# Kernel tuning notes

Measured on AMD Instinct MI355X. Metric: run time of the kernel, lower is better.

The kernel has to match this reference:

```python
import jax, jax.numpy as jnp
import numpy as np

B, T = 64, 64
H = 256
CLIP = 0.2


def _conv(x, W, b, s):
    y = jax.lax.conv_general_dilated(x, W, (s, s), 'VALID',
                                     dimension_numbers=('NHWC', 'HWIO', 'NHWC'))
    return jax.nn.leaky_relu(y + b, negative_slope=0.2)


def _lstm(x, Wk, Wr, b):
    # keras LSTM, gate order i,f,g,o; x: (B,T,256) -> (B,T,256)
    h0 = jnp.zeros((x.shape[0], H), x.dtype)

    def step(carry, xt):
        h, c = carry
        z = xt @ Wk + h @ Wr + b
        i, f, g, o = jnp.split(z, 4, axis=-1)
        c = jax.nn.sigmoid(f) * c + jax.nn.sigmoid(i) * jnp.tanh(g)
        h = jax.nn.sigmoid(o) * jnp.tanh(c)
        return (h, c), h

    _, hs = jax.lax.scan(step, (h0, h0), jnp.swapaxes(x, 0, 1))
    return jnp.swapaxes(hs, 0, 1)


def setup_inputs():
    key = jax.random.key(0)
    ks = jax.random.split(key, 24)
    s = 0.05
    x = jax.random.normal(ks[0], (B, T, 13, 8, 8), jnp.float32)
    a_taken = jax.random.randint(ks[1], (B, T), 0, 36)
    mask = jax.random.randint(ks[2], (B, T, 4096), 0, 2).astype(jnp.int32)
    # taken actions must be legal (mask=1), as in real rollouts
    bi = jnp.repeat(jnp.arange(B), T)
    ti = jnp.tile(jnp.arange(T), B)
    mask = mask.at[bi, ti, a_taken.reshape(-1)].set(1)
    lg_prob_old = -jnp.abs(jax.random.normal(ks[3], (B, T), jnp.float32)) - 1.0
    GAE = jax.random.normal(ks[4], (B, T), jnp.float32)
    old_v_pred = jax.random.normal(ks[5], (B, T), jnp.float32)
    returns = jax.random.normal(ks[6], (B, T), jnp.float32)
    return {
        'x': x, 'mask': mask, 'lg_prob_old': lg_prob_old, 'a_taken': a_taken,
        'GAE': GAE, 'old_v_pred': old_v_pred, 'returns': returns,
        'W1': jax.random.normal(ks[7], (2, 2, 8, 16), jnp.float32) * s,
        'b1': jnp.zeros((16,), jnp.float32),
        'W2': jax.random.normal(ks[8], (2, 2, 16, 32), jnp.float32) * s,
        'b2': jnp.zeros((32,), jnp.float32),
        'W3': jax.random.normal(ks[9], (2, 2, 32, 64), jnp.float32) * s,
        'b3': jnp.zeros((64,), jnp.float32),
        'W4': jax.random.normal(ks[10], (1, 1, 64, 128), jnp.float32) * s,
        'b4': jnp.zeros((128,), jnp.float32),
        'lstm_k': jax.random.normal(ks[11], (256, 1024), jnp.float32) * s,
        'lstm_r': jax.random.normal(ks[12], (256, 1024), jnp.float32) * s,
        'lstm_b': jnp.zeros((1024,), jnp.float32),
        'pir_W': jax.random.normal(ks[13], (256, 36), jnp.float32) * s,
        'pir_b': jnp.zeros((36,), jnp.float32),
        'pim_W': jax.random.normal(ks[14], (256, 4096), jnp.float32) * s,
        'pim_b': jnp.zeros((4096,), jnp.float32),
        'v_W': jax.random.normal(ks[15], (256, 1), jnp.float32) * s,
        'v_b': jnp.zeros((1,), jnp.float32),
    }


def reference(x, mask, lg_prob_old, a_taken, GAE, old_v_pred, returns,
              W1, b1, W2, b2, W3, b3, W4, b4,
              lstm_k, lstm_r, lstm_b, pir_W, pir_b, pim_W, pim_b, v_W, v_b):
    Bn, Tn = x.shape[0], x.shape[1]
    h = x.reshape(Bn * Tn, 13, 8, 8)  # NHWC: H=13, W=8, C=8
    h = _conv(h, W1, b1, 2)  # (BT,6,4,16)
    h = _conv(h, W2, b2, 1)  # (BT,5,3,32)
    h = _conv(h, W3, b3, 2)  # (BT,2,1,64)
    h = _conv(h, W4, b4, 1)  # (BT,2,1,128)
    # keras Flatten(data_format='channels_first') permutes dim1 to last then flattens
    h = jnp.transpose(h, (0, 2, 3, 1)).reshape(Bn, Tn, -1)  # (B,T,256)
    lstm = _lstm(h, lstm_k, lstm_r, lstm_b).reshape(-1, H)  # (BT,256)

    pir = jax.nn.softmax(lstm @ pir_W + pir_b, axis=-1)  # (BT,36)
    maskf = mask.reshape(-1, 4096).astype(jnp.float32)
    pim = jax.nn.softmax(lstm @ pim_W + pim_b, axis=-1) * maskf
    scale = jnp.sum(pim, axis=1, keepdims=True)
    pim = pim / jnp.where(scale > 0, scale, jnp.ones_like(scale))  # (BT,4096)
    vpred = lstm @ v_W + v_b  # (BT,1)

    lg_old = lg_prob_old.reshape(-1)
    a = a_taken.reshape(-1)
    gae = GAE.reshape(-1)
    ovp = old_v_pred.reshape(-1)
    ret = returns.reshape(-1)
    gae = (gae - jnp.mean(gae)) / (jnp.std(gae) + 1e-8)

    t = jnp.arange(a.shape[0])
    p = jnp.where(t % 2 == 0, pir[t, a], pim[t, a])  # alternating heads
    lg_new = jnp.log(p)
    rt = jnp.exp(lg_new - lg_old)
    pg1 = -gae * rt
    pg2 = -gae * jnp.clip(rt, 1.0 - CLIP, 1.0 + CLIP)
    pg_loss = jnp.mean(jnp.maximum(pg1, pg2))

    # faithful to original TF: (BT,1) vpred broadcast against (BT,) -> (BT,BT)
    vpredclipped = ovp + jnp.clip(vpred - ovp, -CLIP, CLIP)
    vf1 = jnp.square(vpred - ret)
    vf2 = jnp.square(vpredclipped - ret)
    vf_loss = 0.5 * jnp.mean(jnp.maximum(vf1, vf2))

    pim_e = pim + (1.0 - maskf)
    entropy = -jnp.sum(pir * jnp.log(pir)) - jnp.sum(pim_e * jnp.log(pim_e))
    loss = pg_loss - entropy + vf_loss
    return (loss, pg_loss, entropy, vf_loss)
```

## Files before the change

kernel.cpp:

```cpp
#include <hip/hip_runtime.h>

typedef unsigned short u16;
typedef unsigned int   u32;

#define BT   4096
#define TSEQ 64
#define NB   64

typedef __attribute__((ext_vector_type(8))) short  short8;
typedef __attribute__((ext_vector_type(4))) float  f32x4;
typedef __attribute__((ext_vector_type(2))) _Float16 h2;

__device__ __forceinline__ float bf(u16 v) {
    u32 u = ((u32)v) << 16;
    return __builtin_bit_cast(float, u);
}
__device__ __forceinline__ u16 f2b(float f) {
    u32 u = __builtin_bit_cast(u32, f);
    return (u16)((u + 0x7fffu + ((u >> 16) & 1u)) >> 16);
}
__device__ __forceinline__ float lrelu(float x) { return x > 0.f ? x : 0.2f * x; }
__device__ __forceinline__ h2 i2h(int v) { return __builtin_bit_cast(h2, v); }
__device__ __forceinline__ float dot2(int hbits, int wbits, float acc) {
#if __has_builtin(__builtin_amdgcn_fdot2)
    return __builtin_amdgcn_fdot2(i2h(hbits), i2h(wbits), acc, false);
#else
    h2 a = i2h(hbits), b = i2h(wbits);
    return acc + (float)a.x * (float)b.x + (float)a.y * (float)b.y;
#endif
}
__device__ __forceinline__ float fsigm(float x) { return 1.f / (1.f + __expf(-x)); }
__device__ __forceinline__ float ftanh(float x) { return 1.f - 2.f / (__expf(2.f * x) + 1.f); }
__device__ __forceinline__ float ldf(const void* p, int i, int f32) {
    return f32 ? ((const float*)p)[i] : bf(((const u16*)p)[i]);
}
__device__ __forceinline__ u16 ldb(const void* p, int i, int f32) {
    return f32 ? f2b(((const float*)p)[i]) : ((const u16*)p)[i];
}

struct PrepPtrs {
    const void *x, *W1, *b1, *W2, *b2, *W3, *b3, *W4, *b4;
    const void *Wr, *Wk, *Wpim, *Wpir, *Wv;
    const u16* probe;
    u16 *featbf, *PF, *PBk, *PBpim, *PBpir;
    float* scal; int* flag;
};

#define PACK_BLKS 6208
#define CONV_BLKS 2048

__global__ __launch_bounds__(256) void prep_kernel(PrepPtrs P)
{
    const int bid = blockIdx.x, tid = threadIdx.x;
    const int lane = tid & 63;
    u16 pv = P.probe[2 * lane];
    int e = (pv >> 7) & 0xFF;
    unsigned long long m = __ballot(pv == 0 || (e >= 100 && e <= 130));
    const int f32 = (__popcll(m) < 48) ? 1 : 0;

    if (bid == 0 && tid < 32) { P.scal[tid] = 0.f; if (tid == 0) *P.flag = f32; }

    if (bid < PACK_BLKS) {
        const int blk = bid;
        if (blk < 1024) {
            int gid = blk * 256 + tid;
            int k = gid >> 10, col = gid & 1023;
            float f = ldf(P.Wr, gid, f32);
            _Float16 h = (_Float16)f;
            P.PF[((size_t)(k >> 3) * 1024 + col) * 8 + (k & 7)] =
                __builtin_bit_cast(unsigned short, h);
        } else if (blk < 2048) {
            int gid = (blk - 1024) * 256 + tid;
            int k = gid >> 10, col = gid & 1023;
            P.PBk[((((size_t)(k >> 5) << 10) + col) * 4 + ((k >> 3) & 3)) * 8 + (k & 7)] =
                ldb(P.Wk, gid, f32);
        } else if (blk < 6144) {
            int gid = (blk - 2048) * 256 + tid;
            int k = gid >> 12, col = gid & 4095;
            P.PBpim[((((size_t)(k >> 5) << 12) + col) * 4 + ((k >> 3) & 3)) * 8 + (k & 7)] =
                ldb(P.Wpim, gid, f32);
        } else {
            int gid = (blk - 6144) * 256 + tid;
            int k = gid >> 6, col = gid & 63;
            u16 v = 0;
            if (col < 36)      v = ldb(P.Wpir, k * 36 + col, f32);
            else if (col == 36) v = ldb(P.Wv, k, f32);
            P.PBpir[(((size_t)(k >> 5) * 64 + col) * 4 + ((k >> 3) & 3)) * 8 + (k & 7)] = v;
        }
        return;
    }

    __shared__ __align__(16) u16 wl[19184];
    __shared__ float xs[2][832];
    __shared__ float c1[2][384];
    __shared__ float c2[2][480];
    __shared__ float c3[2][128];
    const int pair = bid - PACK_BLKS;
    const int sub = tid >> 7, stid = tid & 127;
    const int bt = pair * 2 + sub;

    {
        const void* sp[8] = {P.W1, P.b1, P.W2, P.b2, P.W3, P.b3, P.W4, P.b4};
        const int   sn[8] = {512, 16, 2048, 32, 8192, 64, 8192, 128};
        int o = 0;
        for (int s = 0; s < 8; s++) {
            for (int i = tid; i < sn[s]; i += 256) wl[o + i] = ldb(sp[s], i, f32);
            o += sn[s];
        }
    }
    for (int i = stid; i < 832; i += 128) xs[sub][i] = ldf(P.x, bt * 832 + i, f32);
    __syncthreads();

    for (int idx = stid; idx < 96; idx += 128) {
        int pos = idx >> 2, g = idx & 3;
        int oh = pos >> 2, ow = pos & 3;
        float a0 = bf(wl[512 + g * 4]), a1 = bf(wl[513 + g * 4]),
              a2 = bf(wl[514 + g * 4]), a3 = bf(wl[515 + g * 4]);
        for (int kh = 0; kh < 2; kh++)
            for (int kw = 0; kw < 2; kw++)
#pragma unroll
                for (int ic = 0; ic < 8; ic++) {
                    float xv = xs[sub][(2 * oh + kh) * 64 + (2 * ow + kw) * 8 + ic];
                    ushort4 w = *(const ushort4*)&wl[((kh * 2 + kw) * 8 + ic) * 16 + g * 4];
                    a0 += xv * bf(w.x); a1 += xv * bf(w.y);
                    a2 += xv * bf(w.z); a3 += xv * bf(w.w);
                }
        c1[sub][pos * 16 + g * 4]     = lrelu(a0);
        c1[sub][pos * 16 + g * 4 + 1] = lrelu(a1);
        c1[sub][pos * 16 + g * 4 + 2] = lrelu(a2);
        c1[sub][pos * 16 + g * 4 + 3] = lrelu(a3);
    }
    __syncthreads();

    for (int idx = stid; idx < 120; idx += 128) {
        int pos = idx >> 3, g = idx & 7;
        int oh = pos / 3, ow = pos % 3;
        float a0 = bf(wl[2576 + g * 4]), a1 = bf(wl[2577 + g * 4]),
              a2 = bf(wl[2578 + g * 4]), a3 = bf(wl[2579 + g * 4]);
        for (int kh = 0; kh < 2; kh++)
            for (int kw = 0; kw < 2; kw++)
#pragma unroll
                for (int ic = 0; ic < 16; ic++) {
                    float xv = c1[sub][((oh + kh) * 4 + (ow + kw)) * 16 + ic];
                    ushort4 w = *(const ushort4*)&wl[528 + ((kh * 2 + kw) * 16 + ic) * 32 + g * 4];
                    a0 += xv * bf(w.x); a1 += xv * bf(w.y);
                    a2 += xv * bf(w.z); a3 += xv * bf(w.w);
                }
        c2[sub][pos * 32 + g * 4]     = lrelu(a0);
        c2[sub][pos * 32 + g * 4 + 1] = lrelu(a1);
        c2[sub][pos * 32 + g * 4 + 2] = lrelu(a2);
        c2[sub][pos * 32 + g * 4 + 3] = lrelu(a3);
    }
    __syncthreads();

    for (int idx = stid; idx < 32; idx += 128) {
        int oh = idx >> 4, g = idx & 15;
        float a0 = bf(wl[10800 + g * 4]), a1 = bf(wl[10801 + g * 4]),
              a2 = bf(wl[10802 + g * 4]), a3 = bf(wl[10803 + g * 4]);
        for (int kh = 0; kh < 2; kh++)
            for (int kw = 0; kw < 2; kw++)
#pragma unroll
                for (int ic = 0; ic < 32; ic++) {
                    float xv = c2[sub][((2 * oh + kh) * 3 + kw) * 32 + ic];
                    ushort4 w = *(const ushort4*)&wl[2608 + ((kh * 2 + kw) * 32 + ic) * 64 + g * 4];
                    a0 += xv * bf(w.x); a1 += xv * bf(w.y);
                    a2 += xv * bf(w.z); a3 += xv * bf(w.w);
                }
        c3[sub][oh * 64 + g * 4]     = lrelu(a0);
        c3[sub][oh * 64 + g * 4 + 1] = lrelu(a1);
        c3[sub][oh * 64 + g * 4 + 2] = lrelu(a2);
        c3[sub][oh * 64 + g * 4 + 3] = lrelu(a3);
    }
    __syncthreads();

    for (int idx = stid; idx < 64; idx += 128) {
        int oh = idx >> 5, g = idx & 31;
        float a0 = bf(wl[19056 + g * 4]), a1 = bf(wl[19057 + g * 4]),
              a2 = bf(wl[19058 + g * 4]), a3 = bf(wl[19059 + g * 4]);
#pragma unroll
        for (int ic = 0; ic < 64; ic++) {
            float xv = c3[sub][oh * 64 + ic];
            ushort4 w = *(const ushort4*)&wl[10864 + ic * 128 + g * 4];
            a0 += xv * bf(w.x); a1 += xv * bf(w.y);
            a2 += xv * bf(w.z); a3 += xv * bf(w.w);
        }
        P.featbf[bt * 256 + (g * 4 + 0) * 2 + oh] = f2b(lrelu(a0));
        P.featbf[bt * 256 + (g * 4 + 1) * 2 + oh] = f2b(lrelu(a1));
        P.featbf[bt * 256 + (g * 4 + 2) * 2 + oh] = f2b(lrelu(a2));
        P.featbf[bt * 256 + (g * 4 + 3) * 2 + oh] = f2b(lrelu(a3));
    }
}

__global__ __launch_bounds__(256) void gemm_zx(
    const u16* __restrict__ Abf, const u16* __restrict__ PB,
    const void* __restrict__ bias, const int* __restrict__ flag,
    float* __restrict__ out)
{
    __shared__ __align__(16) u16 As[16 * 264];
    const int mb = blockIdx.y, nb = blockIdx.x, tid = threadIdx.x;
    const int f32 = *flag;
    const int m0 = mb * 16;
    {
        int row = tid >> 4, part = tid & 15;
        const f32x4* src = (const f32x4*)&Abf[(size_t)(m0 + row) * 256 + part * 16];
        f32x4 v0 = src[0], v1 = src[1];
        *(f32x4*)&As[row * 264 + part * 16] = v0;
        *(f32x4*)&As[row * 264 + part * 16 + 8] = v1;
    }
    __syncthreads();
    const int wv = tid >> 6, lane = tid & 63;
    const int colw = lane & 15, q = lane >> 4;
    const int n = nb * 64 + wv * 16 + colw;
    f32x4 acc = {0.f, 0.f, 0.f, 0.f};
#pragma unroll
    for (int kt = 0; kt < 8; kt++) {
        short8 a = *(const short8*)&As[colw * 264 + kt * 32 + q * 8];
        short8 b = *(const short8*)&PB[((((size_t)kt << 10) + n) * 4 + q) * 8];
        acc = __builtin_amdgcn_mfma_f32_16x16x32_bf16(a, b, acc, 0, 0, 0);
    }
    const float bj = ldf(bias, n, f32);
#pragma unroll
    for (int r = 0; r < 4; r++) {
        int row = q * 4 + r;
        out[(size_t)(m0 + row) * 1024 + n] = acc[r] + bj;
    }
}

#define NPRE 18
#define NLDS 7
#define NSTR (32 - NPRE - NLDS)
__global__ __launch_bounds__(1024)
__attribute__((amdgpu_waves_per_eu(4, 4)))
void lstm_kernel(
    const float* __restrict__ zx, const u16* __restrict__ PF,
    u16* __restrict__ hseqbf)
{
    __shared__ float zp[1024];
    __shared__ __align__(16) u16 h16[256];
    __shared__ u16 hist[TSEQ * 256];
    __shared__ __align__(16) int4 wlds[NLDS * 1024];
    const int b = blockIdx.x, tid = threadIdx.x;
    float c = 0.f;
    const int4* Pw = (const int4*)PF;

    int4 wr[NPRE];
#pragma unroll
    for (int j = 0; j < NPRE; j++) wr[j] = Pw[j * 1024 + tid];
#pragma unroll
    for (int j = 0; j < NLDS; j++) wlds[j * 1024 + tid] = Pw[(NPRE + j) * 1024 + tid];
    if (tid < 256) h16[tid] = 0;
    __syncthreads();

    for (int t = 0; t < TSEQ; t++) {
        int4 ws[NSTR];
#pragma unroll
        for (int j = 0; j < NSTR; j++) ws[j] = Pw[(NPRE + NLDS + j) * 1024 + tid];
        float zxv = zx[(size_t)(b * TSEQ + t) * 1024 + tid];

        float a0 = 0.f, a1 = 0.f, a2 = 0.f, a3 = 0.f;
#pragma unroll
        for (int j = 0; j < NPRE; j++) {
            int4 hv = *(const int4*)&h16[j * 8];
            a0 = dot2(hv.x, wr[j].x, a0);
            a1 = dot2(hv.y, wr[j].y, a1);
            a2 = dot2(hv.z, wr[j].z, a2);
            a3 = dot2(hv.w, wr[j].w, a3);
        }
#pragma unroll
        for (int j = 0; j < NLDS; j++) {
            int4 hv = *(const int4*)&h16[(NPRE + j) * 8];
            int4 w = wlds[j * 1024 + tid];
            a0 = dot2(hv.x, w.x, a0);
            a1 = dot2(hv.y, w.y, a1);
            a2 = dot2(hv.z, w.z, a2);
            a3 = dot2(hv.w, w.w, a3);
        }
#pragma unroll
        for (int j = 0; j < NSTR; j++) {
            int4 hv = *(const int4*)&h16[(NPRE + NLDS + j) * 8];
            a0 = dot2(hv.x, ws[j].x, a0);
            a1 = dot2(hv.y, ws[j].y, a1);
            a2 = dot2(hv.z, ws[j].z, a2);
            a3 = dot2(hv.w, ws[j].w, a3);
        }
        zp[tid] = ((a0 + a1) + (a2 + a3)) + zxv;
        __syncthreads();
        if (tid < 256) {
            float ai = zp[tid], af = zp[256 + tid], ag = zp[512 + tid], ao = zp[768 + tid];
            float ig = fsigm(ai), fg = fsigm(af), og = fsigm(ao);
            float gg = ftanh(ag);
            c = fg * c + ig * gg;
            float h = og * ftanh(c);
            h16[tid] = __builtin_bit_cast(unsigned short, (_Float16)h);
            hist[t * 256 + tid] = f2b(h);
        }
        __syncthreads();
    }
    for (int i = tid; i < TSEQ * 256; i += 1024)
        hseqbf[(size_t)b * (TSEQ * 256) + i] = hist[i];
}

__global__ __launch_bounds__(256) void heads_kernel(
    const u16* __restrict__ Abf,
    const u16* __restrict__ PBpir, const u16* __restrict__ PBpim,
    const void* __restrict__ pir_b, const void* __restrict__ v_b,
    const void* __restrict__ pim_b, const int* __restrict__ flag,
    const int* __restrict__ mask, const int* __restrict__ a_taken,
    float* __restrict__ entpir, float* __restrict__ ppira, float* __restrict__ vpred,
    float* __restrict__ partS, float* __restrict__ partU, float* __restrict__ za)
{
    __shared__ __align__(16) u16 As[64 * 264];
    __shared__ float redS[4][16], redU[4][16];
    const int tid = threadIdx.x;
    const int wv = tid >> 6, lane = tid & 63;
    const int colw = lane & 15, q = lane >> 4;
    const int f32 = *flag;

    if (blockIdx.x < 64) {
        const int m0 = blockIdx.x * 64;
        for (int idx = tid; idx < 1024; idx += 256) {
            int row = idx >> 4, part = idx & 15;
            const f32x4* src = (const f32x4*)&Abf[(size_t)(m0 + row) * 256 + part * 16];
            f32x4 v0 = src[0], v1 = src[1];
            *(f32x4*)&As[row * 264 + part * 16] = v0;
            *(f32x4*)&As[row * 264 + part * 16 + 8] = v1;
        }
        __syncthreads();
        f32x4 acc[4];
#pragma unroll
        for (int nt = 0; nt < 4; nt++) acc[nt] = (f32x4){0.f, 0.f, 0.f, 0.f};
#pragma unroll
        for (int kt = 0; kt < 8; kt++) {
            short8 a = *(const short8*)&As[(wv * 16 + colw) * 264 + kt * 32 + q * 8];
#pragma unroll
            for (int nt = 0; nt < 4; nt++) {
                short8 b = *(const short8*)&PBpir[((((size_t)kt * 64) + nt * 16 + colw) * 4 + q) * 8];
                acc[nt] = __builtin_amdgcn_mfma_f32_16x16x32_bf16(a, b, acc[nt], 0, 0, 0);
            }
        }
        float* zq = (float*)&As[wv * 4224];
#pragma unroll
        for (int nt = 0; nt < 4; nt++) {
            int col = nt * 16 + colw;
            float bj = (col < 36) ? ldf(pir_b, col, f32)
                                  : (col == 36 ? ldf(v_b, 0, f32) : 0.f);
#pragma unroll
            for (int r = 0; r < 4; r++)
                zq[(q * 4 + r) * 65 + col] = acc[nt][r] + bj;
        }
        if (lane < 16) {
            int R = m0 + wv * 16 + lane;
            const float* zrow = &zq[lane * 65];
            float Z = 0.f, U = 0.f;
            for (int cc = 0; cc < 36; cc++) {
                float z = zrow[cc];
                float ev = __expf(z);
                Z += ev; U += ev * z;
            }
            entpir[R] = logf(Z) - U / Z;
            ppira[R]  = __expf(zrow[a_taken[R]]) / Z;
            vpred[R]  = zrow[36];
        }
        return;
    }
    const int b2 = blockIdx.x - 64;
    const int nb = b2 & 63, mb = b2 >> 6;
    const int m0 = mb * 16;
    {
        int row = tid >> 4, part = tid & 15;
        const f32x4* src = (const f32x4*)&Abf[(size_t)(m0 + row) * 256 + part * 16];
        f32x4 v0 = src[0], v1 = src[1];
        *(f32x4*)&As[row * 264 + part * 16] = v0;
        *(f32x4*)&As[row * 264 + part * 16 + 8] = v1;
    }
    __syncthreads();
    const int n = nb * 64 + wv * 16 + colw;
    f32x4 acc = {0.f, 0.f, 0.f, 0.f};
#pragma unroll
    for (int kt = 0; kt < 8; kt++) {
        short8 a = *(const short8*)&As[colw * 264 + kt * 32 + q * 8];
        short8 b = *(const short8*)&PBpim[((((size_t)kt << 12) + n) * 4 + q) * 8];
        acc = __builtin_amdgcn_mfma_f32_16x16x32_bf16(a, b, acc, 0, 0, 0);
    }
    const float bj = ldf(pim_b, n, f32);
    float sv[4], uv[4];
#pragma unroll
    for (int r = 0; r < 4; r++) {
        int row = m0 + q * 4 + r;
        float z = acc[r] + bj;
        int mm = mask[(size_t)row * 4096 + n];
        float ev = __expf(z);
        sv[r] = mm ? ev : 0.f;
        uv[r] = mm ? ev * z : 0.f;
        if (n == a_taken[row]) za[row] = z;
    }
#pragma unroll
    for (int r = 0; r < 4; r++) {
        for (int off = 1; off < 16; off <<= 1) {
            sv[r] += __shfl_xor(sv[r], off, 16);
            uv[r] += __shfl_xor(uv[r], off, 16);
        }
        if (colw == 0) { redS[wv][q * 4 + r] = sv[r]; redU[wv][q * 4 + r] = uv[r]; }
    }
    __syncthreads();
    if (tid < 16) {
        float S = redS[0][tid] + redS[1][tid] + redS[2][tid] + redS[3][tid];
        float U = redU[0][tid] + redU[1][tid] + redU[2][tid] + redU[3][tid];
        partS[(size_t)(m0 + tid) * 64 + nb] = S;
        partU[(size_t)(m0 + tid) * 64 + nb] = U;
    }
}

#define TAIL_BLOCKS (16 + 256)
__global__ __launch_bounds__(256) void tail_kernel(
    const float* __restrict__ partS, const float* __restrict__ partU,
    const float* __restrict__ za,
    const float* __restrict__ entpir, const float* __restrict__ ppira,
    const float* __restrict__ vpred,
    const void* __restrict__ lgold, const void* __restrict__ gae,
    const void* __restrict__ ovp, const void* __restrict__ ret,
    float* __restrict__ scal, const int* __restrict__ flag,
    void* __restrict__ out)
{
    const int bid = blockIdx.x, tid = threadIdx.x;
    const int f32 = *flag;
    __shared__ float sh[8];
    __shared__ float mst[2];
    if (bid < 16) {
        const int r = bid * 256 + tid;
        float S = 0.f, U = 0.f;
#pragma unroll
        for (int t2 = 0; t2 < 64; t2++) {
            S += partS[(size_t)r * 64 + t2];
            U += partU[(size_t)r * 64 + t2];
        }
        float entpim = logf(S) - U / S;
        float ppima = __expf(za[r]) / S;
        float s = 0.f, s2 = 0.f;
        if (f32) {
            const float* gp = (const float*)gae;
            for (int i = tid; i < BT; i += 256) { float v = gp[i]; s += v; s2 += v * v; }
        } else {
            const u16* gp = (const u16*)gae;
            for (int i = tid; i < BT; i += 256) { float v = bf(gp[i]); s += v; s2 += v * v; }
        }
        for (int off = 32; off; off >>= 1) {
            s += __shfl_down(s, off, 64); s2 += __shfl_down(s2, off, 64);
        }
        if ((tid & 63) == 0) { sh[tid >> 6] = s; sh[4 + (tid >> 6)] = s2; }
        __syncthreads();
        if (tid == 0) {
            float Sa = sh[0] + sh[1] + sh[2] + sh[3];
            float S2a = sh[4] + sh[5] + sh[6] + sh[7];
            float mean = Sa / (float)BT;
            float var = S2a / (float)BT - mean * mean;
            mst[0] = mean; mst[1] = sqrtf(fmaxf(var, 0.f));
        }
        __syncthreads();
        float mean = mst[0], sd = mst[1];
        float p = (r & 1) ? ppima : ppira[r];
        float ln = logf(p);
        float rt = __expf(ln - ldf(lgold, r, f32));
        float g = (ldf(gae, r, f32) - mean) / (sd + 1e-8f);
        float rtc = fminf(fmaxf(rt, 0.8f), 1.2f);
        float pg = fmaxf(-g * rt, -g * rtc);
        float e12 = entpir[r] + entpim;
        for (int off = 32; off; off >>= 1) {
            pg += __shfl_down(pg, off, 64);
            e12 += __shfl_down(e12, off, 64);
        }
        if ((tid & 63) == 0) {
            atomicAdd(&scal[2], pg);
            atomicAdd(&scal[3], e12);
        }
    } else {
        const int i0 = (bid - 16) * 16;
        float s = 0.f;
        if (f32) {
            const float* rp = (const float*)ret;
            const float* op = (const float*)ovp;
            for (int rr = 0; rr < 16; rr++) {
                float vp = vpred[i0 + rr];
                for (int j = tid; j < BT; j += 256) {
                    float r2 = rp[j], o = op[j];
                    float d = fminf(fmaxf(vp - o, -0.2f), 0.2f);
                    float v1 = vp - r2;    v1 *= v1;
                    float v2 = o + d - r2; v2 *= v2;
                    s += fmaxf(v1, v2);
                }
            }
        } else {
            const u16* rp = (const u16*)ret;
            const u16* op = (const u16*)ovp;
            for (int rr = 0; rr < 16; rr++) {
                float vp = vpred[i0 + rr];
                for (int j = tid; j < BT; j += 256) {
                    float r2 = bf(rp[j]), o = bf(op[j]);
                    float d = fminf(fmaxf(vp - o, -0.2f), 0.2f);
                    float v1 = vp - r2;    v1 *= v1;
                    float v2 = o + d - r2; v2 *= v2;
                    s += fmaxf(v1, v2);
                }
            }
        }
        for (int off = 32; off; off >>= 1) s += __shfl_down(s, off, 64);
        if ((tid & 63) == 0) sh[tid >> 6] = s;
        __syncthreads();
        if (tid == 0) atomicAdd(&scal[5], sh[0] + sh[1] + sh[2] + sh[3]);
    }
    __threadfence();
    __syncthreads();
    if (tid == 0) {
        unsigned old = atomicAdd((unsigned int*)&scal[8], 1u);
        if (old == TAIL_BLOCKS - 1) {
            __threadfence();
            float pgs = atomicAdd(&scal[2], 0.f);
            float ents = atomicAdd(&scal[3], 0.f);
            float vfs = atomicAdd(&scal[5], 0.f);
            float pg = pgs / (float)BT;
            float vf = 0.5f * vfs / ((float)BT * (float)BT);
            float loss = pg - ents + vf;
            if (f32) {
                float* o = (float*)out;
                o[0] = loss; o[1] = pg; o[2] = ents; o[3] = vf;
            } else {
                u16* o = (u16*)out;
                o[0] = f2b(loss); o[1] = f2b(pg); o[2] = f2b(ents); o[3] = f2b(vf);
            }
        }
    }
}

extern "C" void kernel_launch(void* const* d_in, const int* in_sizes, int n_in,
                              void* d_out, int out_size, void* d_ws, size_t ws_size,
                              hipStream_t stream)
{
    const int* mask = (const int*)d_in[1];
    const int* a_tk = (const int*)d_in[3];

    float* p = (float*)d_ws;
    u16*   featbf = (u16*)p;            p += 524288;
    float* zx     = p;                  p += 4194304;
    u16*   hseqbf = (u16*)p;            p += 524288;
    u16*   PF     = (u16*)p;            p += 131072;
    u16*   PBk    = (u16*)p;            p += 131072;
    u16*   PBpim  = (u16*)p;            p += 524288;
    u16*   PBpir  = (u16*)p;            p += 8192;
    float* scal   = p;                  p += 32;
    int*   flag   = (int*)p;            p += 4;
    float* partS  = p;                  p += 262144;
    float* partU  = p;                  p += 262144;
    float* za     = p;                  p += 4096;
    float* entpir = p;                  p += 4096;
    float* ppira  = p;                  p += 4096;
    float* vpred  = p;                  p += 4096;

    PrepPtrs P;
    P.x = d_in[0];
    P.W1 = d_in[7];  P.b1 = d_in[8];
    P.W2 = d_in[9];  P.b2 = d_in[10];
    P.W3 = d_in[11]; P.b3 = d_in[12];
    P.W4 = d_in[13]; P.b4 = d_in[14];
    P.Wk = d_in[15]; P.Wr = d_in[16];
    P.Wpir = d_in[18]; P.Wpim = d_in[20]; P.Wv = d_in[22];
    P.probe = (const u16*)d_in[15];
    P.featbf = featbf; P.PF = PF; P.PBk = PBk; P.PBpim = PBpim; P.PBpir = PBpir;
    P.scal = scal; P.flag = flag;

    prep_kernel<<<PACK_BLKS + CONV_BLKS, 256, 0, stream>>>(P);
    gemm_zx<<<dim3(16, 256), 256, 0, stream>>>(featbf, PBk, d_in[17], flag, zx);
    lstm_kernel<<<NB, 1024, 0, stream>>>(zx, PF, hseqbf);
    heads_kernel<<<64 + 64 * 256, 256, 0, stream>>>(
        hseqbf, PBpir, PBpim, d_in[19], d_in[23], d_in[21], flag, mask, a_tk,
        entpir, ppira, vpred, partS, partU, za);
    tail_kernel<<<TAIL_BLOCKS, 256, 0, stream>>>(
        partS, partU, za, entpir, ppira, vpred,
        d_in[2], d_in[4], d_in[5], d_in[6], scal, flag, (void*)d_out);
}
```

Baseline: 516.2 us.

## Vectorize weight packing and split heads kernel with 32-row pim tiles

The weight-packing blocks now have each thread gather eight k-values and write them with a single 16-byte store, cutting the pack block count eightfold. The combined heads kernel is split into a separate pir kernel and a pim kernel. In the pim kernel each block handles 32 rows instead of 16, so every loaded B fragment feeds two MFMAs and the number of blocks is halved. This adds one kernel launch and raises register use per thread, and the gather loads in the packer are strided.

```diff
diff --git a/kernel.cpp b/kernel.cpp
--- a/kernel.cpp
+++ b/kernel.cpp
@@ -46,7 +46,7 @@
     float* scal; int* flag;
 };
 
-#define PACK_BLKS 6208
+#define PACK_BLKS 776
 #define CONV_BLKS 2048
 
 __global__ __launch_bounds__(256) void prep_kernel(PrepPtrs P)
@@ -61,31 +61,41 @@
     if (bid == 0 && tid < 32) { P.scal[tid] = 0.f; if (tid == 0) *P.flag = f32; }
 
     if (bid < PACK_BLKS) {
-        const int blk = bid;
-        if (blk < 1024) {
-            int gid = blk * 256 + tid;
-            int k = gid >> 10, col = gid & 1023;
-            float f = ldf(P.Wr, gid, f32);
-            _Float16 h = (_Float16)f;
-            P.PF[((size_t)(k >> 3) * 1024 + col) * 8 + (k & 7)] =
-                __builtin_bit_cast(unsigned short, h);
-        } else if (blk < 2048) {
-            int gid = (blk - 1024) * 256 + tid;
-            int k = gid >> 10, col = gid & 1023;
-            P.PBk[((((size_t)(k >> 5) << 10) + col) * 4 + ((k >> 3) & 3)) * 8 + (k & 7)] =
-                ldb(P.Wk, gid, f32);
-        } else if (blk < 6144) {
-            int gid = (blk - 2048) * 256 + tid;
-            int k = gid >> 12, col = gid & 4095;
-            P.PBpim[((((size_t)(k >> 5) << 12) + col) * 4 + ((k >> 3) & 3)) * 8 + (k & 7)] =
-                ldb(P.Wpim, gid, f32);
+        u16 t8[8];
+        if (bid < 128) {
+            int gid = bid * 256 + tid;
+            int col = gid & 1023, oct = gid >> 10;
+#pragma unroll
+            for (int j = 0; j < 8; j++) {
+                float f = ldf(P.Wr, (oct * 8 + j) * 1024 + col, f32);
+                _Float16 h = (_Float16)f;
+                t8[j] = __builtin_bit_cast(unsigned short, h);
+            }
+            *(int4*)&P.PF[((size_t)oct * 1024 + col) * 8] = *(int4*)t8;
+        } else if (bid < 256) {
+            int gid = (bid - 128) * 256 + tid;
+            int col = gid & 1023, oct = gid >> 10;
+#pragma unroll
+            for (int j = 0; j < 8; j++) t8[j] = ldb(P.Wk, (oct * 8 + j) * 1024 + col, f32);
+            *(int4*)&P.PBk[((((size_t)(oct >> 2) << 10) + col) * 4 + (oct & 3)) * 8] = *(int4*)t8;
+        } else if (bid < 768) {
+            int gid = (bid - 256) * 256 + tid;
+            int col = gid & 4095, oct = gid >> 12;
+#pragma unroll
+            for (int j = 0; j < 8; j++) t8[j] = ldb(P.Wpim, (size_t)(oct * 8 + j) * 4096 + col, f32);
+            *(int4*)&P.PBpim[((((size_t)(oct >> 2) << 12) + col) * 4 + (oct & 3)) * 8] = *(int4*)t8;
         } else {
-            int gid = (blk - 6144) * 256 + tid;
-            int k = gid >> 6, col = gid & 63;
-            u16 v = 0;
-            if (col < 36)      v = ldb(P.Wpir, k * 36 + col, f32);
-            else if (col == 36) v = ldb(P.Wv, k, f32);
-            P.PBpir[(((size_t)(k >> 5) * 64 + col) * 4 + ((k >> 3) & 3)) * 8 + (k & 7)] = v;
+            int gid = (bid - 768) * 256 + tid;
+            int col = gid & 63, oct = gid >> 6;
+#pragma unroll
+            for (int j = 0; j < 8; j++) {
+                int k = oct * 8 + j;
+                u16 v = 0;
+                if (col < 36)       v = ldb(P.Wpir, k * 36 + col, f32);
+                else if (col == 36) v = ldb(P.Wv, k, f32);
+                t8[j] = v;
+            }
+            *(int4*)&P.PBpir[(((size_t)(oct >> 2) * 64 + col) * 4 + (oct & 3)) * 8] = *(int4*)t8;
         }
         return;
     }
@@ -300,110 +310,125 @@
         hseqbf[(size_t)b * (TSEQ * 256) + i] = hist[i];
 }
 
-__global__ __launch_bounds__(256) void heads_kernel(
-    const u16* __restrict__ Abf,
-    const u16* __restrict__ PBpir, const u16* __restrict__ PBpim,
+__global__ __launch_bounds__(256) void pir_kernel(
+    const u16* __restrict__ Abf, const u16* __restrict__ PB,
     const void* __restrict__ pir_b, const void* __restrict__ v_b,
-    const void* __restrict__ pim_b, const int* __restrict__ flag,
-    const int* __restrict__ mask, const int* __restrict__ a_taken,
-    float* __restrict__ entpir, float* __restrict__ ppira, float* __restrict__ vpred,
-    float* __restrict__ partS, float* __restrict__ partU, float* __restrict__ za)
+    const int* __restrict__ flag, const int* __restrict__ a_taken,
+    float* __restrict__ entpir, float* __restrict__ ppira, float* __restrict__ vpred)
 {
     __shared__ __align__(16) u16 As[64 * 264];
-    __shared__ float redS[4][16], redU[4][16];
     const int tid = threadIdx.x;
     const int wv = tid >> 6, lane = tid & 63;
     const int colw = lane & 15, q = lane >> 4;
     const int f32 = *flag;
-
-    if (blockIdx.x < 64) {
-        const int m0 = blockIdx.x * 64;
-        for (int idx = tid; idx < 1024; idx += 256) {
-            int row = idx >> 4, part = idx & 15;
-            const f32x4* src = (const f32x4*)&Abf[(size_t)(m0 + row) * 256 + part * 16];
-            f32x4 v0 = src[0], v1 = src[1];
-            *(f32x4*)&As[row * 264 + part * 16] = v0;
-            *(f32x4*)&As[row * 264 + part * 16 + 8] = v1;
-        }
-        __syncthreads();
-        f32x4 acc[4];
-#pragma unroll
-        for (int nt = 0; nt < 4; nt++) acc[nt] = (f32x4){0.f, 0.f, 0.f, 0.f};
-#pragma unroll
-        for (int kt = 0; kt < 8; kt++) {
-            short8 a = *(const short8*)&As[(wv * 16 + colw) * 264 + kt * 32 + q * 8];
-#pragma unroll
-            for (int nt = 0; nt < 4; nt++) {
-                short8 b = *(const short8*)&PBpir[((((size_t)kt * 64) + nt * 16 + colw) * 4 + q) * 8];
-                acc[nt] = __builtin_amdgcn_mfma_f32_16x16x32_bf16(a, b, acc[nt], 0, 0, 0);
-            }
-        }
-        float* zq = (float*)&As[wv * 4224];
-#pragma unroll
-        for (int nt = 0; nt < 4; nt++) {
-            int col = nt * 16 + colw;
-            float bj = (col < 36) ? ldf(pir_b, col, f32)
-                                  : (col == 36 ? ldf(v_b, 0, f32) : 0.f);
-#pragma unroll
-            for (int r = 0; r < 4; r++)
-                zq[(q * 4 + r) * 65 + col] = acc[nt][r] + bj;
-        }
-        if (lane < 16) {
-            int R = m0 + wv * 16 + lane;
-            const float* zrow = &zq[lane * 65];
-            float Z = 0.f, U = 0.f;
-            for (int cc = 0; cc < 36; cc++) {
-                float z = zrow[cc];
-                float ev = __expf(z);
-                Z += ev; U += ev * z;
-            }
-            entpir[R] = logf(Z) - U / Z;
-            ppira[R]  = __expf(zrow[a_taken[R]]) / Z;
-            vpred[R]  = zrow[36];
-        }
-        return;
-    }
-    const int b2 = blockIdx.x - 64;
-    const int nb = b2 & 63, mb = b2 >> 6;
-    const int m0 = mb * 16;
-    {
-        int row = tid >> 4, part = tid & 15;
+    const int m0 = blockIdx.x * 64;
+
+    for (int idx = tid; idx < 1024; idx += 256) {
+        int row = idx >> 4, part = idx & 15;
         const f32x4* src = (const f32x4*)&Abf[(size_t)(m0 + row) * 256 + part * 16];
         f32x4 v0 = src[0], v1 = src[1];
         *(f32x4*)&As[row * 264 + part * 16] = v0;
         *(f32x4*)&As[row * 264 + part * 16 + 8] = v1;
     }
     __syncthreads();
+    f32x4 acc[4];
+#pragma unroll
+    for (int nt = 0; nt < 4; nt++) acc[nt] = (f32x4){0.f, 0.f, 0.f, 0.f};
+#pragma unroll
+    for (int kt = 0; kt < 8; kt++) {
+        short8 a = *(const short8*)&As[(wv * 16 + colw) * 264 + kt * 32 + q * 8];
+#pragma unroll
+        for (int nt = 0; nt < 4; nt++) {
+            short8 b = *(const short8*)&PB[((((size_t)kt * 64) + nt * 16 + colw) * 4 + q) * 8];
+            acc[nt] = __builtin_amdgcn_mfma_f32_16x16x32_bf16(a, b, acc[nt], 0, 0, 0);
+        }
+    }
+    float* zq = (float*)&As[wv * 4224];
+#pragma unroll
+    for (int nt = 0; nt < 4; nt++) {
+        int col = nt * 16 + colw;
+        float bj = (col < 36) ? ldf(pir_b, col, f32)
+                              : (col == 36 ? ldf(v_b, 0, f32) : 0.f);
+#pragma unroll
+        for (int r = 0; r < 4; r++)
+            zq[(q * 4 + r) * 65 + col] = acc[nt][r] + bj;
+    }
+    if (lane < 16) {
+        int R = m0 + wv * 16 + lane;
+        const float* zrow = &zq[lane * 65];
+        float Z = 0.f, U = 0.f;
+        for (int cc = 0; cc < 36; cc++) {
+            float z = zrow[cc];
+            float ev = __expf(z);
+            Z += ev; U += ev * z;
+        }
+        entpir[R] = logf(Z) - U / Z;
+        ppira[R]  = __expf(zrow[a_taken[R]]) / Z;
+        vpred[R]  = zrow[36];
+    }
+}
+
+__global__ __launch_bounds__(256) void pim_kernel(
+    const u16* __restrict__ Abf, const u16* __restrict__ PB,
+    const void* __restrict__ pim_b, const int* __restrict__ flag,
+    const int* __restrict__ mask, const int* __restrict__ a_taken,
+    float* __restrict__ partS, float* __restrict__ partU, float* __restrict__ za)
+{
+    __shared__ __align__(16) u16 As[32 * 264];
+    __shared__ float redS[4][32], redU[4][32];
+    const int nb = blockIdx.x, mb = blockIdx.y, tid = threadIdx.x;
+    const int wv = tid >> 6, lane = tid & 63;
+    const int colw = lane & 15, q = lane >> 4;
+    const int f32 = *flag;
+    const int m0 = mb * 32;
+
+    for (int idx = tid; idx < 512; idx += 256) {
+        int row = idx >> 4, part = idx & 15;
+        const f32x4* src = (const f32x4*)&Abf[(size_t)(m0 + row) * 256 + part * 16];
+        f32x4 v0 = src[0], v1 = src[1];
+        *(f32x4*)&As[row * 264 + part * 16] = v0;
+        *(f32x4*)&As[row * 264 + part * 16 + 8] = v1;
+    }
+    __syncthreads();
     const int n = nb * 64 + wv * 16 + colw;
-    f32x4 acc = {0.f, 0.f, 0.f, 0.f};
+    f32x4 acc0 = {0.f, 0.f, 0.f, 0.f}, acc1 = {0.f, 0.f, 0.f, 0.f};
 #pragma unroll
     for (int kt = 0; kt < 8; kt++) {
-        short8 a = *(const short8*)&As[colw * 264 + kt * 32 + q * 8];
-        short8 b = *(const short8*)&PBpim[((((size_t)kt << 12) + n) * 4 + q) * 8];
-        acc = __builtin_amdgcn_mfma_f32_16x16x32_bf16(a, b, acc, 0, 0, 0);
+        short8 b = *(const short8*)&PB[((((size_t)kt << 12) + n) * 4 + q) * 8];
+        short8 a0 = *(const short8*)&As[colw * 264 + kt * 32 + q * 8];
+        short8 a1 = *(const short8*)&As[(16 + colw) * 264 + kt * 32 + q * 8];
+        acc0 = __builtin_amdgcn_mfma_f32_16x16x32_bf16(a0, b, acc0, 0, 0, 0);
+        acc1 = __builtin_amdgcn_mfma_f32_16x16x32_bf16(a1, b, acc1, 0, 0, 0);
     }
     const float bj = ldf(pim_b, n, f32);
-    float sv[4], uv[4];
-#pragma unroll
-    for (int r = 0; r < 4; r++) {
-        int row = m0 + q * 4 + r;
-        float z = acc[r] + bj;
-        int mm = mask[(size_t)row * 4096 + n];
-        float ev = __expf(z);
-        sv[r] = mm ? ev : 0.f;
-        uv[r] = mm ? ev * z : 0.f;
-        if (n == a_taken[row]) za[row] = z;
-    }
-#pragma unroll
-    for (int r = 0; r < 4; r++) {
-        for (int off = 1; off < 16; off <<= 1) {
-            sv[r] += __shfl_xor(sv[r], off, 16);
-            uv[r] += __shfl_xor(uv[r], off, 16);
-        }
-        if (colw == 0) { redS[wv][q * 4 + r] = sv[r]; redU[wv][q * 4 + r] = uv[r]; }
-    }
-    __syncthreads();
-    if (tid < 16) {
+#pragma unroll
+    for (int half = 0; half < 2; half++) {
+        const f32x4& acc = half ? acc1 : acc0;
+        float sv[4], uv[4];
+#pragma unroll
+        for (int r = 0; r < 4; r++) {
+            int row = m0 + half * 16 + q * 4 + r;
+            float z = acc[r] + bj;
+            int mm = mask[(size_t)row * 4096 + n];
+            float ev = __expf(z);
+            sv[r] = mm ? ev : 0.f;
+            uv[r] = mm ? ev * z : 0.f;
+            if (n == a_taken[row]) za[row] = z;
+        }
+#pragma unroll
+        for (int r = 0; r < 4; r++) {
+            for (int off = 1; off < 16; off <<= 1) {
+                sv[r] += __shfl_xor(sv[r], off, 16);
+                uv[r] += __shfl_xor(uv[r], off, 16);
+            }
+            if (colw == 0) {
+                redS[wv][half * 16 + q * 4 + r] = sv[r];
+                redU[wv][half * 16 + q * 4 + r] = uv[r];
+            }
+        }
+    }
+    __syncthreads();
+    if (tid < 32) {
         float S = redS[0][tid] + redS[1][tid] + redS[2][tid] + redS[3][tid];
         float U = redU[0][tid] + redU[1][tid] + redU[2][tid] + redU[3][tid];
         partS[(size_t)(m0 + tid) * 64 + nb] = S;
@@ -570,9 +595,10 @@
     prep_kernel<<<PACK_BLKS + CONV_BLKS, 256, 0, stream>>>(P);
     gemm_zx<<<dim3(16, 256), 256, 0, stream>>>(featbf, PBk, d_in[17], flag, zx);
     lstm_kernel<<<NB, 1024, 0, stream>>>(zx, PF, hseqbf);
-    heads_kernel<<<64 + 64 * 256, 256, 0, stream>>>(
-        hseqbf, PBpir, PBpim, d_in[19], d_in[23], d_in[21], flag, mask, a_tk,
-        entpir, ppira, vpred, partS, partU, za);
+    pir_kernel<<<64, 256, 0, stream>>>(hseqbf, PBpir, d_in[19], d_in[23], flag,
+                                       a_tk, entpir, ppira, vpred);
+    pim_kernel<<<dim3(64, 128), 256, 0, stream>>>(hseqbf, PBpim, d_in[21], flag,
+                                                  mask, a_tk, partS, partU, za);
     tail_kernel<<<TAIL_BLOCKS, 256, 0, stream>>>(
         partS, partU, za, entpir, ppira, vpred,
         d_in[2], d_in[4], d_in[5], d_in[6], scal, flag, (void*)d_out);
```

After: 488.8 us. 5.3% less time.
